# Performance work log

Measured on AMD Instinct MI355X. Metric: run time of the kernel, lower is better.

Reference implementation:

```python
import jax, jax.numpy as jnp
import numpy as np

N, E = 20000, 320000
IN, OUT, H1, H2 = 256, 32, 8, 1
NEG_SLOPE = 0.2


def _gatv2(x, src, dst, Wsrc, bsrc, Wdst, bdst, attn, Wres, bres, heads, dout):
    n = x.shape[0]
    fs = (x @ Wsrc + bsrc).reshape(n, heads, dout)   # (N,H,D)
    fd = (x @ Wdst + bdst).reshape(n, heads, dout)   # (N,H,D)
    # GATv2: leaky_relu BEFORE the attention dot product
    e = jax.nn.leaky_relu(fs[src] + fd[dst], NEG_SLOPE)      # (E,H,D)
    logits = jnp.einsum('ehd,hd->eh', e, attn)               # (E,H)
    # edge softmax over destination-node segments
    m = jax.ops.segment_max(logits, dst, num_segments=n)     # (N,H)
    ex = jnp.exp(logits - m[dst])
    s = jax.ops.segment_sum(ex, dst, num_segments=n)         # (N,H)
    alpha = ex / s[dst]                                      # (E,H)
    msg = alpha[:, :, None] * fs[src]                        # (E,H,D)
    out = jax.ops.segment_sum(msg, dst, num_segments=n)      # (N,H,D)
    res = (x @ Wres + bres).reshape(n, heads, dout)          # residual (dims differ -> Linear)
    return out + res


def setup_inputs() -> dict:
    key = jax.random.key(0)
    ks = jax.random.split(key, 16)
    sc = lambda fin: 1.0 / np.sqrt(fin)
    d = {}
    d['x'] = jax.random.normal(ks[0], (N, IN), jnp.float32)
    d['src'] = jax.random.randint(ks[1], (E,), 0, N, jnp.int32)
    d['dst'] = jax.random.randint(ks[2], (E,), 0, N, jnp.int32)
    # layer 1: IN -> OUT*H1
    d['Wsrc1'] = jax.random.normal(ks[3], (IN, OUT * H1), jnp.float32) * sc(IN)
    d['bsrc1'] = jnp.zeros((OUT * H1,), jnp.float32)
    d['Wdst1'] = jax.random.normal(ks[4], (IN, OUT * H1), jnp.float32) * sc(IN)
    d['bdst1'] = jnp.zeros((OUT * H1,), jnp.float32)
    d['attn1'] = jax.random.normal(ks[5], (H1, OUT), jnp.float32) * sc(OUT)
    d['Wres1'] = jax.random.normal(ks[6], (IN, OUT * H1), jnp.float32) * sc(IN)
    d['bres1'] = jnp.zeros((OUT * H1,), jnp.float32)
    # layer 2: OUT*H1 -> OUT, 1 head
    D2 = OUT * H1
    d['Wsrc2'] = jax.random.normal(ks[7], (D2, OUT * H2), jnp.float32) * sc(D2)
    d['bsrc2'] = jnp.zeros((OUT * H2,), jnp.float32)
    d['Wdst2'] = jax.random.normal(ks[8], (D2, OUT * H2), jnp.float32) * sc(D2)
    d['bdst2'] = jnp.zeros((OUT * H2,), jnp.float32)
    d['attn2'] = jax.random.normal(ks[9], (H2, OUT), jnp.float32) * sc(OUT)
    d['Wres2'] = jax.random.normal(ks[10], (D2, OUT * H2), jnp.float32) * sc(D2)
    d['bres2'] = jnp.zeros((OUT * H2,), jnp.float32)
    return d


def reference(x, src, dst,
              Wsrc1, bsrc1, Wdst1, bdst1, attn1, Wres1, bres1,
              Wsrc2, bsrc2, Wdst2, bdst2, attn2, Wres2, bres2):
    y = _gatv2(x, src, dst, Wsrc1, bsrc1, Wdst1, bdst1, attn1, Wres1, bres1, H1, OUT)
    y = jax.nn.relu(y)                       # (N, 8, OUT)
    y = y.reshape(x.shape[0], -1)            # (N, 8*OUT)
    y = _gatv2(y, src, dst, Wsrc2, bsrc2, Wdst2, bdst2, attn2, Wres2, bres2, H2, OUT)
    return y                                  # (N, 1, OUT)
```

## Files before the change

### kernel.cpp

```cpp
#include <hip/hip_runtime.h>
#include <hip/hip_bf16.h>

#define N_NODES 20000
#define N_PAD   20096
#define N_EDGES 320000
#define D_IN    256
#define NEG     0.2f
#define MAXDEG  64
#define NSB     64
#define EPSB    5000
#define NBIN    313
#define LOG2E   1.4426950408889634f

typedef __attribute__((ext_vector_type(8))) short short8;
typedef __attribute__((ext_vector_type(4))) float f32x4;
typedef __attribute__((ext_vector_type(4))) unsigned short u16x4;

__device__ __forceinline__ unsigned short f2b(float f) {
    unsigned int u = __float_as_uint(f);
    unsigned int r = (u + 0x7FFFu + ((u >> 16) & 1u)) >> 16;
    return (unsigned short)r;
}
__device__ __forceinline__ float b2f(unsigned short u) {
    union { unsigned int i; float f; } v;
    v.i = ((unsigned int)u) << 16;
    return v.f;
}

__device__ __forceinline__ void gload16(const void* g, void* l) {
    __builtin_amdgcn_global_load_lds((const __attribute__((address_space(1))) void*)g,
                                     (__attribute__((address_space(3))) void*)l, 16, 0, 0);
}

#define PB1 2512
#define PB1B 2560
#define PB2 2656
#define PB3 2720
#define PREP_BLOCKS 2768
__global__ __launch_bounds__(256) void k_prep(
    const float* __restrict__ x, unsigned short* __restrict__ xb,
    const float* __restrict__ Ws1, const float* __restrict__ Wd1, const float* __restrict__ Wr1,
    unsigned short* __restrict__ wt,
    const float* __restrict__ Ws2, const float* __restrict__ Wd2, const float* __restrict__ Wr2,
    unsigned short* __restrict__ wt2,
    const int* __restrict__ dst, int* __restrict__ blockhist,
    unsigned short* __restrict__ yb)
{
    __shared__ float tl[64][65];
    __shared__ int hist[NBIN];
    int bid = blockIdx.x, tid = threadIdx.x;
    if (bid < PB1) {
        int i = bid * 256 + tid;
        int row = i >> 5, c8 = (i & 31) * 8;
        short8 v = {0, 0, 0, 0, 0, 0, 0, 0};
        if (row < N_NODES) {
            float4 a = *reinterpret_cast<const float4*>(x + (size_t)row * 256 + c8);
            float4 b = *reinterpret_cast<const float4*>(x + (size_t)row * 256 + c8 + 4);
            v[0] = (short)f2b(a.x); v[1] = (short)f2b(a.y); v[2] = (short)f2b(a.z); v[3] = (short)f2b(a.w);
            v[4] = (short)f2b(b.x); v[5] = (short)f2b(b.y); v[6] = (short)f2b(b.z); v[7] = (short)f2b(b.w);
        }
        *reinterpret_cast<short8*>(xb + (size_t)row * 256 + c8) = v;
    } else if (bid < PB1B) {
        int b = bid - PB1;
        int mat = b >> 4, tile = b & 15;
        int r0 = (tile >> 2) * 64;
        int c0 = (tile & 3) * 64;
        const float* W = (mat == 0) ? Ws1 : ((mat == 1) ? Wd1 : Wr1);
        int lane = tid & 63, grp = tid >> 6;
#pragma unroll
        for (int pass = 0; pass < 16; ++pass) {
            int kl = pass * 4 + grp;
            tl[kl][lane] = W[(size_t)(r0 + kl) * 256 + c0 + lane];
        }
        __syncthreads();
#pragma unroll
        for (int pass = 0; pass < 16; ++pass) {
            int nl = pass * 4 + grp;
            wt[(size_t)(mat * 256 + c0 + nl) * 256 + r0 + lane] = f2b(tl[lane][nl]);
        }
    } else if (bid < PB2) {
        int n = bid - PB1B, k = tid;
        const float* W = (n < 32) ? Ws2 : ((n < 64) ? Wd2 : Wr2);
        int c = n & 31;
        wt2[(size_t)n * 256 + (k ^ ((n & 7) << 3))] = f2b(W[(size_t)k * 32 + c]);
    } else if (bid < PB3) {
        int blk = bid - PB2;
        for (int b = tid; b < NBIN; b += 256) hist[b] = 0;
        __syncthreads();
        for (int it = 0; it < 20; ++it) {
            int li = it * 256 + tid;
            if (li < EPSB) atomicAdd(&hist[dst[blk * EPSB + li] >> 6], 1);
        }
        __syncthreads();
        for (int b = tid; b < NBIN; b += 256) blockhist[blk * NBIN + b] = hist[b];
    } else {
        int j = (bid - PB3) * 256 + tid;
        ((unsigned int*)(yb + (size_t)N_NODES * 256))[j] = 0u;
    }
}

__global__ __launch_bounds__(320) void k_pass3(
    const int* __restrict__ src, const int* __restrict__ dst,
    const int* __restrict__ blockhist,
    unsigned long long* __restrict__ sorted,
    int* __restrict__ binbase_g, int* __restrict__ bintotal_g)
{
    __shared__ int tmp[320];
    __shared__ int binbase[NBIN];
    __shared__ int rank[NBIN];
    int blk = blockIdx.x, tid = threadIdx.x;
    int mystart = 0, total = 0;
    if (tid < NBIN) {
        for (int b = 0; b < NSB; ++b) {
            int v = blockhist[b * NBIN + tid];
            total += v;
            if (b < blk) mystart += v;
        }
    }
    tmp[tid] = (tid < NBIN) ? total : 0;
    __syncthreads();
    for (int off = 1; off < 320; off <<= 1) {
        int v = (tid >= off) ? tmp[tid - off] : 0;
        __syncthreads();
        tmp[tid] += v;
        __syncthreads();
    }
    if (tid < NBIN) {
        int excl = tmp[tid] - total;
        binbase[tid] = excl;
        rank[tid] = mystart;
        if (blk == 0) { binbase_g[tid] = excl; bintotal_g[tid] = total; }
    }
    __syncthreads();
    for (int it = 0; it < 16; ++it) {
        int li = it * 320 + tid;
        if (li < EPSB) {
            int e = blk * EPSB + li;
            int d = dst[e];
            int b = d >> 6;
            int r = atomicAdd(&rank[b], 1);
            sorted[binbase[b] + r] = ((unsigned long long)(unsigned)d << 32) | (unsigned)src[e];
        }
    }
}

#define GEMM1_BLOCKS 1884
#define PASS4_BLOCKS 313
__global__ __launch_bounds__(256) void k_gemm_l1_mfma(
    const unsigned short* __restrict__ xb,
    const unsigned short* __restrict__ wt,
    const float* __restrict__ bs, const float* __restrict__ bd, const float* __restrict__ br,
    unsigned short* __restrict__ fs, unsigned short* __restrict__ fd, unsigned short* __restrict__ res,
    const unsigned long long* __restrict__ sorted,
    const int* __restrict__ binbase_g, const int* __restrict__ bintotal_g,
    int* __restrict__ colp, int* __restrict__ cnt)
{
    __shared__ __align__(16) unsigned short SH[12288];
    int t = threadIdx.x;
    int bid = blockIdx.x;

    if (bid >= GEMM1_BLOCKS) {
        int* ch = (int*)SH;
        int nb2 = bid - GEMM1_BLOCKS;
        if (t < 64) ch[t] = 0;
        __syncthreads();
        int base = binbase_g[nb2], tot = bintotal_g[nb2];
        for (int i = t; i < tot; i += 256) {
            unsigned long long p = sorted[base + i];
            int d = (int)(p >> 32);
            int s = (int)(p & 0xffffffffULL);
            int r = atomicAdd(&ch[d & 63], 1);
            if (r < MAXDEG) colp[(size_t)d * MAXDEG + r] = s;
        }
        __syncthreads();
        int node = nb2 * 64 + t;
        if (t < 64 && node < N_NODES) cnt[node] = ch[t];
        return;
    }

    int lane = t & 63, w = t >> 6;
    const int q = 235, r = 4;
    int xcd = bid & 7, slot = bid >> 3;
    int wg = (xcd < r ? xcd * (q + 1) : r * (q + 1) + (xcd - r) * q) + slot;
    int mb = wg / 6, nb = wg % 6;
    int row0 = mb * 64;
    int which = nb >> 1;
    int col0 = (nb & 1) * 128;
    int ncol0 = nb * 128;
    unsigned short* out = (which == 0) ? fs : ((which == 1) ? fd : res);
    const float* bias   = (which == 0) ? bs : ((which == 1) ? bd : br);

    auto stage = [&](int buf, int k0) {
        char* base = (char*)SH + buf * 12288;
        {
            int c = t, row = c >> 2, kc = (c & 3) * 8;
            gload16(xb + (size_t)(row0 + row) * 256 + k0 + kc, base + c * 16);
        }
#pragma unroll
        for (int r2 = 0; r2 < 2; r2++) {
            int c = r2 * 256 + t, row = c >> 2, kc = (c & 3) * 8;
            gload16(wt + (size_t)(ncol0 + row) * 256 + k0 + kc, base + 4096 + c * 16);
        }
    };

    f32x4 acc[4][2] = {};

    stage(0, 0);
    __syncthreads();
    int cur = 0;
#pragma unroll
    for (int it = 0; it < 8; ++it) {
        if (it < 7) stage(cur ^ 1, (it + 1) * 32);
        const char* Ab = (const char*)SH + cur * 12288;
        const char* Bb = Ab + 4096;
        short8 a[4], b[2];
#pragma unroll
        for (int m = 0; m < 4; m++)
            a[m] = *reinterpret_cast<const short8*>(Ab + ((m * 16 + (lane & 15)) * 64 + (lane >> 4) * 16));
#pragma unroll
        for (int n = 0; n < 2; n++)
            b[n] = *reinterpret_cast<const short8*>(Bb + ((w * 32 + n * 16 + (lane & 15)) * 64 + (lane >> 4) * 16));
#pragma unroll
        for (int m = 0; m < 4; m++)
#pragma unroll
            for (int n = 0; n < 2; n++)
                acc[m][n] = __builtin_amdgcn_mfma_f32_16x16x32_bf16(a[m], b[n], acc[m][n], 0, 0, 0);
        __syncthreads();
        cur ^= 1;
    }

    int cgrp = lane >> 4, ccol = lane & 15;
    float bvals[2];
#pragma unroll
    for (int n = 0; n < 2; n++) bvals[n] = bias[col0 + w * 32 + n * 16 + ccol];

#pragma unroll
    for (int m = 0; m < 4; m++)
#pragma unroll
        for (int n = 0; n < 2; n++)
#pragma unroll
            for (int q2 = 0; q2 < 4; q2++) {
                int lr = m * 16 + cgrp * 4 + q2;
                int cb = (w * 32 + n * 16 + ccol) * 2;
                int addr = lr * 256 + (cb ^ (cgrp << 5));
                *(unsigned short*)((char*)SH + addr) = f2b(acc[m][n][q2] + bvals[n]);
            }
    __syncthreads();
#pragma unroll
    for (int it = 0; it < 4; it++) {
        int lr = it * 16 + (t >> 4);
        int cb = (t & 15) * 16;
        short8 v = *(const short8*)((const char*)SH + (lr * 256 + (cb ^ (((lr >> 2) & 3) << 5))));
        int gr = row0 + lr;
        if (gr < N_NODES)
            *reinterpret_cast<short8*>(out + (size_t)gr * 256 + col0 + (t & 15) * 8) = v;
    }
}

__global__ __launch_bounds__(64) void k_gather_l1(
    const int* __restrict__ cnt, const int* __restrict__ colp,
    const unsigned short* __restrict__ fs1, const unsigned short* __restrict__ fd1,
    const unsigned short* __restrict__ res1, const float* __restrict__ attn1,
    unsigned short* __restrict__ y)
{
    __shared__ int slds[MAXDEG + 8];
    int n = blockIdx.x;
    int l = threadIdx.x;
    int deg = cnt[n];
    if (deg > MAXDEG) deg = MAXDEG;
    slds[l] = (l < deg) ? colp[(size_t)n * MAXDEG + l] : 0;
    if (l < 8) slds[MAXDEG + l] = 0;
    __syncthreads();

    u16x4 fdv4 = *reinterpret_cast<const u16x4*>(fd1 + (size_t)n * 256 + l * 4);
    float fdv0 = b2f(fdv4[0]), fdv1 = b2f(fdv4[1]), fdv2 = b2f(fdv4[2]), fdv3 = b2f(fdv4[3]);
    float4 attv = *reinterpret_cast<const float4*>(attn1 + l * 4);
    float at0 = attv.x * LOG2E, at1 = attv.y * LOG2E, at2 = attv.z * LOG2E, at3 = attv.w * LOG2E;

    float sA = 0.f, aA0 = 0.f, aA1 = 0.f, aA2 = 0.f, aA3 = 0.f;
    float sB = 0.f, aB0 = 0.f, aB1 = 0.f, aB2 = 0.f, aB3 = 0.f;

    u16x4 f0 = *reinterpret_cast<const u16x4*>(fs1 + (size_t)slds[0] * 256 + l * 4);
    u16x4 f1 = *reinterpret_cast<const u16x4*>(fs1 + (size_t)slds[1] * 256 + l * 4);
    u16x4 f2 = *reinterpret_cast<const u16x4*>(fs1 + (size_t)slds[2] * 256 + l * 4);
    u16x4 f3 = *reinterpret_cast<const u16x4*>(fs1 + (size_t)slds[3] * 256 + l * 4);

    int idx = 0;
    for (; idx + 1 < deg; idx += 2) {
        u16x4 vA = f0, vB = f1;
        f0 = f2; f1 = f3;
        f2 = *reinterpret_cast<const u16x4*>(fs1 + (size_t)slds[idx + 4] * 256 + l * 4);
        f3 = *reinterpret_cast<const u16x4*>(fs1 + (size_t)slds[idx + 5] * 256 + l * 4);

        float xa0 = b2f(vA[0]), xa1 = b2f(vA[1]), xa2 = b2f(vA[2]), xa3 = b2f(vA[3]);
        float ta0 = xa0 + fdv0; ta0 = fmaxf(ta0, NEG * ta0);
        float ta1 = xa1 + fdv1; ta1 = fmaxf(ta1, NEG * ta1);
        float ta2 = xa2 + fdv2; ta2 = fmaxf(ta2, NEG * ta2);
        float ta3 = xa3 + fdv3; ta3 = fmaxf(ta3, NEG * ta3);
        float pA = ta0 * at0 + ta1 * at1 + ta2 * at2 + ta3 * at3;

        float xb0 = b2f(vB[0]), xb1 = b2f(vB[1]), xb2 = b2f(vB[2]), xb3 = b2f(vB[3]);
        float tb0 = xb0 + fdv0; tb0 = fmaxf(tb0, NEG * tb0);
        float tb1 = xb1 + fdv1; tb1 = fmaxf(tb1, NEG * tb1);
        float tb2 = xb2 + fdv2; tb2 = fmaxf(tb2, NEG * tb2);
        float tb3 = xb3 + fdv3; tb3 = fmaxf(tb3, NEG * tb3);
        float pB = tb0 * at0 + tb1 * at1 + tb2 * at2 + tb3 * at3;

        pA += __shfl_xor(pA, 1); pB += __shfl_xor(pB, 1);
        pA += __shfl_xor(pA, 2); pB += __shfl_xor(pB, 2);
        pA += __shfl_xor(pA, 4); pB += __shfl_xor(pB, 4);

        float eA = exp2f(pA);
        sA += eA;
        aA0 += eA * xa0; aA1 += eA * xa1; aA2 += eA * xa2; aA3 += eA * xa3;

        float eB = exp2f(pB);
        sB += eB;
        aB0 += eB * xb0; aB1 += eB * xb1; aB2 += eB * xb2; aB3 += eB * xb3;
    }
    if (idx < deg) {
        float xa0 = b2f(f0[0]), xa1 = b2f(f0[1]), xa2 = b2f(f0[2]), xa3 = b2f(f0[3]);
        float ta0 = xa0 + fdv0; ta0 = fmaxf(ta0, NEG * ta0);
        float ta1 = xa1 + fdv1; ta1 = fmaxf(ta1, NEG * ta1);
        float ta2 = xa2 + fdv2; ta2 = fmaxf(ta2, NEG * ta2);
        float ta3 = xa3 + fdv3; ta3 = fmaxf(ta3, NEG * ta3);
        float pA = ta0 * at0 + ta1 * at1 + ta2 * at2 + ta3 * at3;
        pA += __shfl_xor(pA, 1);
        pA += __shfl_xor(pA, 2);
        pA += __shfl_xor(pA, 4);
        float eA = exp2f(pA);
        sA += eA;
        aA0 += eA * xa0; aA1 += eA * xa1; aA2 += eA * xa2; aA3 += eA * xa3;
    }
    float s  = sA + sB;
    float a0 = aA0 + aB0, a1 = aA1 + aB1, a2 = aA2 + aB2, a3 = aA3 + aB3;

    u16x4 rv4 = *reinterpret_cast<const u16x4*>(res1 + (size_t)n * 256 + l * 4);
    float inv = (s > 0.f) ? 1.f / s : 0.f;
    u16x4 o;
    o[0] = f2b(fmaxf(a0 * inv + b2f(rv4[0]), 0.f));
    o[1] = f2b(fmaxf(a1 * inv + b2f(rv4[1]), 0.f));
    o[2] = f2b(fmaxf(a2 * inv + b2f(rv4[2]), 0.f));
    o[3] = f2b(fmaxf(a3 * inv + b2f(rv4[3]), 0.f));
    *reinterpret_cast<u16x4*>(y + (size_t)n * 256 + l * 4) = o;
}

__global__ __launch_bounds__(256) void k_gemm_l2_mfma(
    const unsigned short* __restrict__ yb,
    const unsigned short* __restrict__ wt2,
    const float* __restrict__ bs, const float* __restrict__ bd, const float* __restrict__ br,
    unsigned short* __restrict__ fs2, unsigned short* __restrict__ fd2, unsigned short* __restrict__ res2)
{
    __shared__ __align__(16) unsigned short Bs[96 * 256];
    __shared__ __align__(16) unsigned short As[2][64 * 32];
    int t = threadIdx.x;
    int lane = t & 63, w = t >> 6;
    int row0 = blockIdx.x * 64;

    auto stage_a = [&](int buf, int k0) {
        int c = t;
        int row = c >> 2, kc = (c & 3) * 8;
        gload16(yb + (size_t)(row0 + row) * 256 + k0 + kc, (char*)As[buf] + c * 16);
    };

#pragma unroll
    for (int i = 0; i < 12; i++) {
        int c = i * 256 + t;
        gload16(wt2 + (size_t)c * 8, (char*)Bs + (size_t)c * 16);
    }
    stage_a(0, 0);
    __syncthreads();

    f32x4 acc[6] = {};
    int arow0 = w * 16;
    int cur = 0;

#pragma unroll
    for (int it = 0; it < 8; ++it) {
        if (it < 7) stage_a(cur ^ 1, (it + 1) * 32);
        short8 a = *reinterpret_cast<const short8*>((const char*)As[cur] + ((arow0 + (lane & 15)) * 64 + (lane >> 4) * 16));
        short8 b[6];
#pragma unroll
        for (int n = 0; n < 6; n++) {
            int brow = n * 16 + (lane & 15);
            int kbyte = (it * 32 + (lane >> 4) * 8) * 2;
            b[n] = *reinterpret_cast<const short8*>((const char*)Bs + (brow * 512 + (kbyte ^ ((brow & 7) << 4))));
        }
#pragma unroll
        for (int n = 0; n < 6; n++)
            acc[n] = __builtin_amdgcn_mfma_f32_16x16x32_bf16(a, b[n], acc[n], 0, 0, 0);
        __syncthreads();
        cur ^= 1;
    }

    int cgrp = lane >> 4, ccol = lane & 15;
#pragma unroll
    for (int n = 0; n < 6; n++) {
        int which = n >> 1;
        int cc = (n & 1) * 16 + ccol;
        unsigned short* out = (which == 0) ? fs2 : ((which == 1) ? fd2 : res2);
        const float* bias   = (which == 0) ? bs  : ((which == 1) ? bd  : br);
        float bv = bias[cc];
        int rbase = row0 + arow0 + cgrp * 4;
#pragma unroll
        for (int q2 = 0; q2 < 4; q2++) {
            int rr = rbase + q2;
            if (rr < N_NODES) out[(size_t)rr * 32 + cc] = f2b(acc[n][q2] + bv);
        }
    }
}

__global__ __launch_bounds__(64) void k_gather_l2(
    const int* __restrict__ cnt, const int* __restrict__ colp,
    const unsigned short* __restrict__ fs2, const unsigned short* __restrict__ fd2,
    const unsigned short* __restrict__ res2, const float* __restrict__ attn2,
    float* __restrict__ out)
{
    __shared__ int slds[MAXDEG + 8];
    int n = blockIdx.x;
    int l = threadIdx.x;
    int d = l & 31, h = l >> 5;
    int deg = cnt[n];
    if (deg > MAXDEG) deg = MAXDEG;
    slds[l] = (l < deg) ? colp[(size_t)n * MAXDEG + l] : 0;
    if (l < 8) slds[MAXDEG + l] = 0;
    __syncthreads();

    float fdv = b2f(fd2[(size_t)n * 32 + d]);
    float att = attn2[d] * LOG2E;
    float s = 0.f, acc = 0.f;
    float fv_next = b2f(fs2[(size_t)slds[h] * 32 + d]);
    for (int i = h; i < deg; i += 2) {
        float fv = fv_next;
        fv_next = b2f(fs2[(size_t)slds[i + 2] * 32 + d]);
        float t0 = fv + fdv; t0 = fmaxf(t0, NEG * t0);
        float p = t0 * att;
        p += __shfl_xor(p, 1);
        p += __shfl_xor(p, 2);
        p += __shfl_xor(p, 4);
        p += __shfl_xor(p, 8);
        p += __shfl_xor(p, 16);
        float e = exp2f(p);
        s += e;
        acc += e * fv;
    }
    float st = s + __shfl_xor(s, 32);
    float at = acc + __shfl_xor(acc, 32);
    if (l < 32) {
        float rv = b2f(res2[(size_t)n * 32 + d]);
        float inv = (st > 0.f) ? 1.f / st : 0.f;
        out[(size_t)n * 32 + d] = at * inv + rv;
    }
}

extern "C" void kernel_launch(void* const* d_in, const int* in_sizes, int n_in,
                              void* d_out, int out_size, void* d_ws, size_t ws_size,
                              hipStream_t stream)
{
    const float* x   = (const float*)d_in[0];
    const int*   src = (const int*)d_in[1];
    const int*   dst = (const int*)d_in[2];
    const float* Ws1 = (const float*)d_in[3];
    const float* bs1 = (const float*)d_in[4];
    const float* Wd1 = (const float*)d_in[5];
    const float* bd1 = (const float*)d_in[6];
    const float* at1 = (const float*)d_in[7];
    const float* Wr1 = (const float*)d_in[8];
    const float* br1 = (const float*)d_in[9];
    const float* Ws2 = (const float*)d_in[10];
    const float* bs2 = (const float*)d_in[11];
    const float* Wd2 = (const float*)d_in[12];
    const float* bd2 = (const float*)d_in[13];
    const float* at2 = (const float*)d_in[14];
    const float* Wr2 = (const float*)d_in[15];
    const float* br2 = (const float*)d_in[16];
    float* out = (float*)d_out;

    char* w = (char*)d_ws;
    size_t off = 0;
    auto alloc = [&](size_t bytes) { void* p = w + off; off += (bytes + 255) & ~(size_t)255; return p; };
    int*   cnt       = (int*)  alloc((size_t)N_NODES * 4);
    int*   colp      = (int*)  alloc((size_t)N_NODES * MAXDEG * 4);
    int*   blockhist = (int*)  alloc((size_t)NSB * NBIN * 4);
    int*   bintotal  = (int*)  alloc((size_t)NBIN * 4);
    int*   binbase   = (int*)  alloc((size_t)NBIN * 4);
    unsigned long long* sorted = (unsigned long long*)alloc((size_t)N_EDGES * 8);
    unsigned short* fs1 = (unsigned short*)alloc((size_t)N_NODES * 256 * 2);
    unsigned short* fd1 = (unsigned short*)alloc((size_t)N_NODES * 256 * 2);
    unsigned short* res1= (unsigned short*)alloc((size_t)N_NODES * 256 * 2);
    unsigned short* fs2 = (unsigned short*)alloc((size_t)N_NODES * 32 * 2);
    unsigned short* fd2 = (unsigned short*)alloc((size_t)N_NODES * 32 * 2);
    unsigned short* res2= (unsigned short*)alloc((size_t)N_NODES * 32 * 2);
    unsigned short* xb  = (unsigned short*)alloc((size_t)N_PAD * 256 * 2);
    unsigned short* yb  = (unsigned short*)alloc((size_t)N_PAD * 256 * 2);
    unsigned short* wt  = (unsigned short*)alloc((size_t)768 * 256 * 2);
    unsigned short* wt2 = (unsigned short*)alloc((size_t)96 * 256 * 2);
    (void)ws_size; (void)in_sizes; (void)n_in; (void)out_size;

    k_prep<<<PREP_BLOCKS, 256, 0, stream>>>(x, xb, Ws1, Wd1, Wr1, wt, Ws2, Wd2, Wr2, wt2,
                                            dst, blockhist, yb);
    k_pass3<<<NSB, 320, 0, stream>>>(src, dst, blockhist, sorted, binbase, bintotal);
    k_gemm_l1_mfma<<<GEMM1_BLOCKS + PASS4_BLOCKS, 256, 0, stream>>>(
        xb, wt, bs1, bd1, br1, fs1, fd1, res1, sorted, binbase, bintotal, colp, cnt);
    k_gather_l1<<<N_NODES, 64, 0, stream>>>(cnt, colp, fs1, fd1, res1, at1, yb);
    k_gemm_l2_mfma<<<N_PAD / 64, 256, 0, stream>>>(yb, wt2, bs2, bd2, br2, fs2, fd2, res2);
    k_gather_l2<<<N_NODES, 64, 0, stream>>>(cnt, colp, fs2, fd2, res2, at2, out);
}
```

Before: 102.7 us.

## Replace binned counting-sort CSR build with direct global-atomic bucketing

Drops the histogram and scatter-sort kernels (k_pass3 and the sorted buffer) and builds the per-destination neighbour lists directly. Each edge does a global atomicAdd on cnt[dst] and writes src into colp, with cnt zeroed inside k_prep. This removes one kernel launch and a serial dependency stage ahead of the GEMM. In exchange it relies on global atomics with random addresses and makes neighbour order nondeterministic, which can change floating-point summation order.

```diff
diff --git a/kernel.cpp b/kernel.cpp
--- a/kernel.cpp
+++ b/kernel.cpp
@@ -7,9 +7,6 @@
 #define D_IN    256
 #define NEG     0.2f
 #define MAXDEG  64
-#define NSB     64
-#define EPSB    5000
-#define NBIN    313
 #define LOG2E   1.4426950408889634f
 
 typedef __attribute__((ext_vector_type(8))) short short8;
@@ -35,19 +32,17 @@
 #define PB1 2512
 #define PB1B 2560
 #define PB2 2656
-#define PB3 2720
-#define PREP_BLOCKS 2768
+#define PB3 2735
+#define PREP_BLOCKS 2783
 __global__ __launch_bounds__(256) void k_prep(
     const float* __restrict__ x, unsigned short* __restrict__ xb,
     const float* __restrict__ Ws1, const float* __restrict__ Wd1, const float* __restrict__ Wr1,
     unsigned short* __restrict__ wt,
     const float* __restrict__ Ws2, const float* __restrict__ Wd2, const float* __restrict__ Wr2,
     unsigned short* __restrict__ wt2,
-    const int* __restrict__ dst, int* __restrict__ blockhist,
-    unsigned short* __restrict__ yb)
+    int* __restrict__ cnt, unsigned short* __restrict__ yb)
 {
     __shared__ float tl[64][65];
-    __shared__ int hist[NBIN];
     int bid = blockIdx.x, tid = threadIdx.x;
     if (bid < PB1) {
         int i = bid * 256 + tid;
@@ -84,97 +79,35 @@
         int c = n & 31;
         wt2[(size_t)n * 256 + (k ^ ((n & 7) << 3))] = f2b(W[(size_t)k * 32 + c]);
     } else if (bid < PB3) {
-        int blk = bid - PB2;
-        for (int b = tid; b < NBIN; b += 256) hist[b] = 0;
-        __syncthreads();
-        for (int it = 0; it < 20; ++it) {
-            int li = it * 256 + tid;
-            if (li < EPSB) atomicAdd(&hist[dst[blk * EPSB + li] >> 6], 1);
-        }
-        __syncthreads();
-        for (int b = tid; b < NBIN; b += 256) blockhist[blk * NBIN + b] = hist[b];
+        int idx = (bid - PB2) * 256 + tid;
+        if (idx < N_NODES) cnt[idx] = 0;
     } else {
         int j = (bid - PB3) * 256 + tid;
         ((unsigned int*)(yb + (size_t)N_NODES * 256))[j] = 0u;
     }
 }
 
-__global__ __launch_bounds__(320) void k_pass3(
-    const int* __restrict__ src, const int* __restrict__ dst,
-    const int* __restrict__ blockhist,
-    unsigned long long* __restrict__ sorted,
-    int* __restrict__ binbase_g, int* __restrict__ bintotal_g)
-{
-    __shared__ int tmp[320];
-    __shared__ int binbase[NBIN];
-    __shared__ int rank[NBIN];
-    int blk = blockIdx.x, tid = threadIdx.x;
-    int mystart = 0, total = 0;
-    if (tid < NBIN) {
-        for (int b = 0; b < NSB; ++b) {
-            int v = blockhist[b * NBIN + tid];
-            total += v;
-            if (b < blk) mystart += v;
-        }
-    }
-    tmp[tid] = (tid < NBIN) ? total : 0;
-    __syncthreads();
-    for (int off = 1; off < 320; off <<= 1) {
-        int v = (tid >= off) ? tmp[tid - off] : 0;
-        __syncthreads();
-        tmp[tid] += v;
-        __syncthreads();
-    }
-    if (tid < NBIN) {
-        int excl = tmp[tid] - total;
-        binbase[tid] = excl;
-        rank[tid] = mystart;
-        if (blk == 0) { binbase_g[tid] = excl; bintotal_g[tid] = total; }
-    }
-    __syncthreads();
-    for (int it = 0; it < 16; ++it) {
-        int li = it * 320 + tid;
-        if (li < EPSB) {
-            int e = blk * EPSB + li;
-            int d = dst[e];
-            int b = d >> 6;
-            int r = atomicAdd(&rank[b], 1);
-            sorted[binbase[b] + r] = ((unsigned long long)(unsigned)d << 32) | (unsigned)src[e];
-        }
-    }
-}
-
 #define GEMM1_BLOCKS 1884
-#define PASS4_BLOCKS 313
+#define BUCKET_BLOCKS 1250
 __global__ __launch_bounds__(256) void k_gemm_l1_mfma(
     const unsigned short* __restrict__ xb,
     const unsigned short* __restrict__ wt,
     const float* __restrict__ bs, const float* __restrict__ bd, const float* __restrict__ br,
     unsigned short* __restrict__ fs, unsigned short* __restrict__ fd, unsigned short* __restrict__ res,
-    const unsigned long long* __restrict__ sorted,
-    const int* __restrict__ binbase_g, const int* __restrict__ bintotal_g,
-    int* __restrict__ colp, int* __restrict__ cnt)
+    const int* __restrict__ src, const int* __restrict__ dst,
+    int* __restrict__ cnt, int* __restrict__ colp)
 {
     __shared__ __align__(16) unsigned short SH[12288];
     int t = threadIdx.x;
     int bid = blockIdx.x;
 
     if (bid >= GEMM1_BLOCKS) {
-        int* ch = (int*)SH;
-        int nb2 = bid - GEMM1_BLOCKS;
-        if (t < 64) ch[t] = 0;
-        __syncthreads();
-        int base = binbase_g[nb2], tot = bintotal_g[nb2];
-        for (int i = t; i < tot; i += 256) {
-            unsigned long long p = sorted[base + i];
-            int d = (int)(p >> 32);
-            int s = (int)(p & 0xffffffffULL);
-            int r = atomicAdd(&ch[d & 63], 1);
-            if (r < MAXDEG) colp[(size_t)d * MAXDEG + r] = s;
-        }
-        __syncthreads();
-        int node = nb2 * 64 + t;
-        if (t < 64 && node < N_NODES) cnt[node] = ch[t];
+        int e = (bid - GEMM1_BLOCKS) * 256 + t;
+        if (e < N_EDGES) {
+            int d = dst[e];
+            int pos = atomicAdd(&cnt[d], 1);
+            if (pos < MAXDEG) colp[(size_t)d * MAXDEG + pos] = src[e];
+        }
         return;
     }
 
@@ -479,12 +412,8 @@
     char* w = (char*)d_ws;
     size_t off = 0;
     auto alloc = [&](size_t bytes) { void* p = w + off; off += (bytes + 255) & ~(size_t)255; return p; };
-    int*   cnt       = (int*)  alloc((size_t)N_NODES * 4);
-    int*   colp      = (int*)  alloc((size_t)N_NODES * MAXDEG * 4);
-    int*   blockhist = (int*)  alloc((size_t)NSB * NBIN * 4);
-    int*   bintotal  = (int*)  alloc((size_t)NBIN * 4);
-    int*   binbase   = (int*)  alloc((size_t)NBIN * 4);
-    unsigned long long* sorted = (unsigned long long*)alloc((size_t)N_EDGES * 8);
+    int*   cnt  = (int*)  alloc((size_t)N_NODES * 4);
+    int*   colp = (int*)  alloc((size_t)N_NODES * MAXDEG * 4);
     unsigned short* fs1 = (unsigned short*)alloc((size_t)N_NODES * 256 * 2);
     unsigned short* fd1 = (unsigned short*)alloc((size_t)N_NODES * 256 * 2);
     unsigned short* res1= (unsigned short*)alloc((size_t)N_NODES * 256 * 2);
@@ -498,10 +427,9 @@
     (void)ws_size; (void)in_sizes; (void)n_in; (void)out_size;
 
     k_prep<<<PREP_BLOCKS, 256, 0, stream>>>(x, xb, Ws1, Wd1, Wr1, wt, Ws2, Wd2, Wr2, wt2,
-                                            dst, blockhist, yb);
-    k_pass3<<<NSB, 320, 0, stream>>>(src, dst, blockhist, sorted, binbase, bintotal);
-    k_gemm_l1_mfma<<<GEMM1_BLOCKS + PASS4_BLOCKS, 256, 0, stream>>>(
-        xb, wt, bs1, bd1, br1, fs1, fd1, res1, sorted, binbase, bintotal, colp, cnt);
+                                            cnt, yb);
+    k_gemm_l1_mfma<<<GEMM1_BLOCKS + BUCKET_BLOCKS, 256, 0, stream>>>(
+        xb, wt, bs1, bd1, br1, fs1, fd1, res1, src, dst, cnt, colp);
     k_gather_l1<<<N_NODES, 64, 0, stream>>>(cnt, colp, fs1, fd1, res1, at1, yb);
     k_gemm_l2_mfma<<<N_PAD / 64, 256, 0, stream>>>(yb, wt2, bs2, bd2, br2, fs2, fd2, res2);
     k_gather_l2<<<N_NODES, 64, 0, stream>>>(cnt, colp, fs2, fd2, res2, at2, out);
```

Result: slower. 107.0 us (+4.2%).
